# Performance work log

Hardware: AMD Instinct MI355X
Metric: run time of the kernel (lower is better)

Reference implementation:

```python
import jax, jax.numpy as jnp
import numpy as np

B, VN, QN, KN = 64, 100, 64, 64
V_DIM, Q_DIM, KG_DIM = 2048, 768, 300
H_DIM, RANK, GLIMPSE = 1024, 32, 2
HD = H_DIM // RANK  # 32


def setup_inputs() -> dict:
    key = jax.random.key(0)
    ks = jax.random.split(key, 10)
    v = jax.random.normal(ks[0], (B, VN, V_DIM), jnp.float32)
    # zero out last 10 regions so the padding mask path is exercised
    v = v.at[:, VN - 10:, :].set(0.0)
    q = jax.random.normal(ks[1], (B, QN, Q_DIM), jnp.float32)
    kg = jax.random.normal(ks[2], (B, KN, KG_DIM), jnp.float32)
    s = lambda d: 1.0 / np.sqrt(d)
    Wv = jax.random.normal(ks[3], (V_DIM, H_DIM), jnp.float32) * s(V_DIM)
    bv = jnp.zeros((H_DIM,), jnp.float32)
    Wq = jax.random.normal(ks[4], (Q_DIM, H_DIM), jnp.float32) * s(Q_DIM)
    bq = jnp.zeros((H_DIM,), jnp.float32)
    Wkg = jax.random.normal(ks[5], (KG_DIM, H_DIM), jnp.float32) * s(KG_DIM)
    bkg = jnp.zeros((H_DIM,), jnp.float32)
    # core tensor (torch init is normal_(); scaled down so softmax isn't saturated)
    T_g = jax.random.normal(ks[6], (1, RANK, HD, HD, HD, GLIMPSE), jnp.float32) * 0.02
    return {"v": v, "q": q, "kg": kg, "Wv": Wv, "bv": bv, "Wq": Wq, "bq": bq,
            "Wkg": Wkg, "bkg": bkg, "T_g": T_g}


def _tri_logits(v, q, kg, Wv, bv, Wq, bq, Wkg, bkg, T_g):
    b, vn = v.shape[:2]
    qn, kn = q.shape[1], kg.shape[1]
    rank, hd, g = T_g.shape[1], T_g.shape[2], T_g.shape[-1]
    fc = lambda x, W, bb: jax.nn.relu(x @ W + bb)  # FCNet (weight-norm Linear + ReLU), eval: no dropout
    # project to h_dim and split into `rank` contiguous chunks of size hd -> [R,B,N,hd]
    vt = jnp.transpose(fc(v, Wv, bv).reshape(b, vn, rank, hd), (2, 0, 1, 3))
    qt = jnp.transpose(fc(q, Wq, bq).reshape(b, qn, rank, hd), (2, 0, 1, 3))
    kt = jnp.transpose(fc(kg, Wkg, bkg).reshape(b, kn, rank, hd), (2, 0, 1, 3))

    def step(acc, xs):
        vr, qr, kr, Tr = xs  # [B,V,hd],[B,Q,hd],[B,K,hd],[hd,hd,hd,g]
        t = jnp.einsum('bvx,xyzg->bvyzg', vr, Tr)
        t = jnp.einsum('bvyzg,bqy->bvqzg', t, qr)
        t = jnp.einsum('bvqzg,bkz->bvqkg', t, kr)
        return acc + t, None

    init = jnp.zeros((b, vn, qn, kn, g), v.dtype)
    logits, _ = jax.lax.scan(step, init, (vt, qt, kt, T_g[0]))
    return logits  # [B,V,Q,K,glimpse]


def reference(v, q, kg, Wv, bv, Wq, bq, Wkg, bkg, T_g):
    b, vn = v.shape[:2]
    qn, kn = q.shape[1], kg.shape[1]
    g = T_g.shape[-1]
    logits = _tri_logits(v, q, kg, Wv, bv, Wq, bq, Wkg, bkg, T_g)
    # mask padded image regions (all-zero feature rows)
    mask = jnp.sum(jnp.abs(v), axis=2) == 0  # [B,V]
    logits = jnp.where(mask[:, :, None, None, None], -jnp.inf, logits)
    # softmax over the flattened V*Q*K axis, per glimpse
    p = jax.nn.softmax(logits.reshape(b, vn * qn * kn, g), axis=1)
    return p.reshape(b, vn, qn, kn, g), logits
```

## Files before the change

### kernel.cpp

```cpp
#include <hip/hip_runtime.h>
#include <cstdint>
#include <math.h>

#define MASK_VAL (-1e30f)

#define Bb   64
#define VN   100
#define QN   64
#define KN   64
#define VD   2048
#define QD   768
#define KGD  300
#define KGP  320
#define HH   1024
#define RR   32
#define HDm  32
#define GG   2
#define NBV  (Bb*VN)
#define LOGN ((size_t)NBV*QN*KN*GG)

typedef _Float16 half_t;
typedef _Float16 f16x8 __attribute__((ext_vector_type(8)));
typedef _Float16 f16x4 __attribute__((ext_vector_type(4)));
typedef float    f32x4 __attribute__((ext_vector_type(4)));

#define MFMA_F16(a,b,c) __builtin_amdgcn_mfma_f32_16x16x32_f16(a,b,c,0,0,0)

#define PN0 13107200
#define PN1 3145728
#define PN2 1310720
#define PN3 2097152
#define PN4 786432
#define PN5 327680
#define PN6 2097152
#define PTOT (PN0+PN1+PN2+PN3+PN4+PN5+PN6)

__device__ inline void fm_decode(long d, int KB, int& row, int& k) {
  int blk = (int)(d >> 9);
  int lc = (int)((d >> 7) & 3), lr = (int)((d >> 3) & 15), h = (int)(d & 7);
  row = (blk / KB) * 16 + lr;
  k   = (blk % KB) * 32 + lc*8 + h;
}

__global__ __launch_bounds__(256) void preproc_kernel(const float* __restrict__ v,
                                                      const float* __restrict__ q,
                                                      const float* __restrict__ kg,
                                                      const float* __restrict__ Wv,
                                                      const float* __restrict__ Wq,
                                                      const float* __restrict__ Wkg,
                                                      const float* __restrict__ Tg,
                                                      half_t* __restrict__ v16,
                                                      half_t* __restrict__ q16,
                                                      half_t* __restrict__ k16,
                                                      half_t* __restrict__ Wvt,
                                                      half_t* __restrict__ Wqt,
                                                      half_t* __restrict__ Wkt,
                                                      half_t* __restrict__ Tpp)
{
  long idx = (long)blockIdx.x*256 + threadIdx.x;
  if (idx >= PTOT) return;
  int row, k;
  if (idx < PN0) { fm_decode(idx, 64, row, k); v16[idx] = (half_t)v[(size_t)row*VD + k]; return; }
  idx -= PN0;
  if (idx < PN1) { fm_decode(idx, 24, row, k); q16[idx] = (half_t)q[(size_t)row*QD + k]; return; }
  idx -= PN1;
  if (idx < PN2) {
    fm_decode(idx, 10, row, k);
    k16[idx] = (half_t)((k < KGD) ? kg[(size_t)row*KGD + k] : 0.f);
    return;
  }
  idx -= PN2;
  if (idx < PN3) { fm_decode(idx, 64, row, k); Wvt[idx] = (half_t)Wv[(size_t)k*HH + row]; return; }
  idx -= PN3;
  if (idx < PN4) { fm_decode(idx, 24, row, k); Wqt[idx] = (half_t)Wq[(size_t)k*HH + row]; return; }
  idx -= PN4;
  if (idx < PN5) {
    fm_decode(idx, 10, row, k);
    Wkt[idx] = (half_t)((k < KGD) ? Wkg[(size_t)k*HH + row] : 0.f);
    return;
  }
  idx -= PN5;
  {
    int r = (int)(idx >> 16), rem = (int)(idx & 65535);
    int cp = rem >> 5, x = rem & 31;
    int y = cp & 31, zg = cp >> 5;
    Tpp[idx + (size_t)0] = (half_t)Tg[((size_t)(r*32 + x) << 11) + y*64 + zg];
  }
}

__global__ __launch_bounds__(256) void mask_kernel(const float* __restrict__ v,
                                                   float* __restrict__ maskv)
{
  int row = blockIdx.x;
  int tid = threadIdx.x;
  const float* src = v + (size_t)row * VD;
  float s = 0.f;
  for (int i = tid; i < VD/4; i += 256) {
    float4 x = *(const float4*)&src[i*4];
    s += fabsf(x.x)+fabsf(x.y)+fabsf(x.z)+fabsf(x.w);
  }
#pragma unroll
  for (int off=32; off; off>>=1) s += __shfl_down(s, off);
  __shared__ float red[4];
  if ((tid & 63) == 0) red[tid>>6] = s;
  __syncthreads();
  if (tid == 0) maskv[row] = ((red[0]+red[1]+red[2]+red[3]) == 0.f) ? 1.f : 0.f;
}

__global__ __launch_bounds__(256) void proj_mfma_kernel(const half_t* __restrict__ A0,
                                                        const half_t* __restrict__ A1,
                                                        const half_t* __restrict__ A2,
                                                        const half_t* __restrict__ W0,
                                                        const half_t* __restrict__ W1,
                                                        const half_t* __restrict__ W2,
                                                        const float* __restrict__ b0p,
                                                        const float* __restrict__ b1p,
                                                        const float* __restrict__ b2p,
                                                        half_t* __restrict__ H0,
                                                        half_t* __restrict__ H1,
                                                        half_t* __restrict__ H2)
{
  int z = blockIdx.z;
  int Mb = (z == 0) ? 100 : 64;
  if ((int)blockIdx.x >= Mb) return;
  const half_t* A  = (z==0) ? A0 : (z==1) ? A1 : A2;
  const half_t* Wt = (z==0) ? W0 : (z==1) ? W1 : W2;
  const float* bias = (z==0) ? b0p : (z==1) ? b1p : b2p;
  half_t* H = (z==0) ? H0 : (z==1) ? H1 : H2;
  int KB = (z==0) ? 64 : (z==1) ? 24 : 10;

  int w = threadIdx.x >> 6, lane = threadIdx.x & 63;
  int mtile = blockIdx.x*4 + w;
  int n0 = blockIdx.y*64;
  int lr = lane & 15, lc = lane >> 4;
  f32x4 acc[4];
#pragma unroll
  for (int nt=0;nt<4;nt++) acc[nt] = (f32x4)(0.f);
  const half_t* abase = A + ((size_t)mtile*KB)*512 + lane*8;
  const half_t* wbase = Wt + ((size_t)(blockIdx.y*4)*KB)*512 + lane*8;
  for (int kb = 0; kb < KB; kb++) {
    f16x8 a = *(const f16x8*)(abase + (size_t)kb*512);
#pragma unroll
    for (int nt = 0; nt < 4; nt++) {
      f16x8 b = *(const f16x8*)(wbase + ((size_t)nt*KB + kb)*512);
      acc[nt] = MFMA_F16(a, b, acc[nt]);
    }
  }
  int m0 = mtile*16;
#pragma unroll
  for (int nt = 0; nt < 4; nt++) {
    float bb = bias[n0 + nt*16 + lr];
#pragma unroll
    for (int j = 0; j < 4; j++) {
      float vv = fmaxf(acc[nt][j] + bb, 0.f);
      H[(size_t)(m0 + lc*4 + j)*HH + n0 + nt*16 + lr] = (half_t)vv;
    }
  }
}

__global__ __launch_bounds__(256) void stageA_mfma_kernel(const half_t* __restrict__ hv,
                                                          const half_t* __restrict__ Tpp,
                                                          half_t* __restrict__ u, int r0)
{
  __shared__ half_t tile[4][16][256];
  int rc = blockIdx.z; int r = r0 + rc;
  int w = threadIdx.x >> 6, lane = threadIdx.x & 63;
  int m0 = blockIdx.x*64 + w*16;
  int n0 = blockIdx.y*256;
  int lr = lane & 15, lc = lane >> 4;
  f16x8 bH = *(const f16x8*)(hv + (size_t)(m0 + lr)*HH + r*HDm + lc*8);
  const half_t* ta = Tpp + ((size_t)r << 16) + (size_t)n0*32 + lr*32 + lc*8;
  half_t* myt = &tile[w][0][0];
#pragma unroll
  for (int t = 0; t < 16; t++) {
    f16x8 aT = *(const f16x8*)(ta + t*512);
    f32x4 d = MFMA_F16(aT, bH, (f32x4)(0.f));
    f16x4 pk;
    pk[0] = (half_t)d[0]; pk[1] = (half_t)d[1];
    pk[2] = (half_t)d[2]; pk[3] = (half_t)d[3];
    int col4 = (t*4 + lc) ^ (lr & 14);
    *(f16x4*)(myt + lr*256 + col4*4) = pk;
  }
  half_t* ub = u + ((size_t)rc*NBV + m0)*2048 + n0;
  int hl = lane >> 5;
  int cc = lane & 31;
#pragma unroll
  for (int i = 0; i < 8; i++) {
    int rrow = i*2 + hl;
    int pc4 = (cc*2) ^ (rrow & 14);
    f16x8 val = *(const f16x8*)(myt + rrow*256 + pc4*4);
    *(f16x8*)(ub + (size_t)rrow*2048 + cc*8) = val;
  }
}

#define WSTRIDE 2080
__global__ __launch_bounds__(256,2) void triBC_mfma_kernel(const half_t* __restrict__ hq,
                                                           const half_t* __restrict__ hk,
                                                           const half_t* __restrict__ u,
                                                           const float* __restrict__ maskv,
                                                           uint32_t* __restrict__ logits16,
                                                           float* __restrict__ pm,
                                                           float* __restrict__ ps,
                                                           int r0, int RC, int isFirst, int isLast)
{
  __shared__ __align__(16) half_t qtf[2][2048];
  __shared__ __align__(16) half_t ktf[2][2048];
  __shared__ __align__(16) half_t wsm[4*2*WSTRIDE];
  int tid = threadIdx.x;
  int w = tid >> 6, lane = tid & 63;
  half_t* wme = wsm + w*(2*WSTRIDE);
  int vt = blockIdx.x, b = blockIdx.y;
  int bv = b*VN + vt*4 + w;
  int lr = lane & 15, lc = lane >> 4;

  f32x4 acc[2][4][4];
#pragma unroll
  for (int g=0;g<2;g++)
#pragma unroll
    for (int mt=0;mt<4;mt++)
#pragma unroll
      for (int nt=0;nt<4;nt++) acc[g][mt][nt] = (f32x4)(0.f);

  int srow = tid >> 2, sch = tid & 3;
  const half_t* qsrc = hq + (size_t)(b*QN + srow)*HH + sch*8;
  const half_t* ksrc = hk + (size_t)(b*KN + srow)*HH + sch*8;
  int sdst = (srow>>4)*512 + ((srow&15) + sch*16)*8;
  const half_t* ulane = u + (size_t)bv*2048 + lr*HDm + lc*8;

  *(f16x8*)&qtf[0][sdst] = *(const f16x8*)(qsrc + r0*HDm);
  *(f16x8*)&ktf[0][sdst] = *(const f16x8*)(ksrc + r0*HDm);
  int rp1 = (RC > 1) ? 1 : 0;
  f16x8 qhold = *(const f16x8*)(qsrc + (r0+rp1)*HDm);
  f16x8 khold = *(const f16x8*)(ksrc + (r0+rp1)*HDm);
  f16x8 ub[4];
#pragma unroll
  for (int nt=0;nt<4;nt++) ub[nt] = *(const f16x8*)(ulane + nt*512);
  asm volatile("s_waitcnt lgkmcnt(0)" ::: "memory");
  __builtin_amdgcn_s_barrier();

  for (int rc = 0; rc < RC; rc++) {
    int bp = rc & 1;
    int rn1 = (rc+1 < RC) ? rc+1 : RC-1;
    int rn2 = (rc+2 < RC) ? rc+2 : RC-1;
    f16x8 qa[4], bk[4];
#pragma unroll
    for (int mt=0;mt<4;mt++) qa[mt] = *(const f16x8*)&qtf[bp][mt*512 + lane*8];
#pragma unroll
    for (int nt=0;nt<4;nt++) bk[nt] = *(const f16x8*)&ktf[bp][nt*512 + lane*8];
    *(f16x8*)&qtf[bp^1][sdst] = qhold;
    *(f16x8*)&ktf[bp^1][sdst] = khold;
    qhold = *(const f16x8*)(qsrc + (r0+rn2)*HDm);
    khold = *(const f16x8*)(ksrc + (r0+rn2)*HDm);
    f16x8 ubN[4];
#pragma unroll
    for (int nt=0;nt<4;nt++)
      ubN[nt] = *(const f16x8*)(ulane + (size_t)rn1*NBV*2048 + nt*512);
#pragma unroll
    for (int nt=0;nt<4;nt++) {
      f32x4 wv[4];
#pragma unroll
      for (int mt=0;mt<4;mt++) wv[mt] = MFMA_F16(qa[mt], ub[nt], (f32x4)(0.f));
#pragma unroll
      for (int mt=0;mt<4;mt++) {
#pragma unroll
        for (int j=0;j<4;j++) {
          int dst = (lr&1)*WSTRIDE + mt*512 + (lc*4 + j + nt*16)*8 + (lr>>1);
          wme[dst] = (half_t)wv[mt][j];
        }
      }
    }
#pragma unroll
    for (int g=0;g<2;g++) {
      f16x8 am[4];
#pragma unroll
      for (int mt=0;mt<4;mt++) am[mt] = *(const f16x8*)&wme[g*WSTRIDE + mt*512 + lane*8];
#pragma unroll
      for (int mt=0;mt<4;mt++)
#pragma unroll
        for (int nt=0;nt<4;nt++)
          acc[g][mt][nt] = MFMA_F16(am[mt], bk[nt], acc[g][mt][nt]);
    }
    asm volatile("s_waitcnt lgkmcnt(0)" ::: "memory");
    __builtin_amdgcn_s_barrier();
#pragma unroll
    for (int nt=0;nt<4;nt++) ub[nt] = ubN[nt];
  }

  float mk = maskv[bv];
  uint32_t* lb16 = logits16 + (size_t)bv*QN*KN;
#pragma unroll
  for (int mt=0;mt<4;mt++)
#pragma unroll
    for (int nt=0;nt<4;nt++)
#pragma unroll
      for (int j=0;j<4;j++) {
        size_t off = (size_t)(mt*16 + lc*4 + j)*KN + nt*16 + lr;
        float g0 = acc[0][mt][nt][j], g1 = acc[1][mt][nt][j];
        if (!isFirst) {
          union { uint32_t u32; half_t h[2]; } pv;
          pv.u32 = lb16[off];
          g0 += (float)pv.h[0]; g1 += (float)pv.h[1];
        }
        if (isLast && mk != 0.f) { g0 = MASK_VAL; g1 = MASK_VAL; }
        union { uint32_t u32; half_t h[2]; } pk;
        pk.h[0] = (half_t)g0; pk.h[1] = (half_t)g1;
        lb16[off] = pk.u32;
        acc[0][mt][nt][j] = g0; acc[1][mt][nt][j] = g1;
      }
  if (isLast) {
#pragma unroll
    for (int g=0; g<2; g++) {
      float mloc = acc[g][0][0][0];
#pragma unroll
      for (int mt=0;mt<4;mt++)
#pragma unroll
        for (int nt=0;nt<4;nt++)
#pragma unroll
          for (int j=0;j<4;j++) mloc = fmaxf(mloc, acc[g][mt][nt][j]);
      float sloc = 0.f;
#pragma unroll
      for (int mt=0;mt<4;mt++)
#pragma unroll
        for (int nt=0;nt<4;nt++)
#pragma unroll
          for (int j=0;j<4;j++) sloc += __expf(acc[g][mt][nt][j] - mloc);
#pragma unroll
      for (int off2=1; off2<64; off2<<=1) {
        float m2 = __shfl_xor(mloc, off2);
        float s2 = __shfl_xor(sloc, off2);
        float mn = fmaxf(mloc, m2);
        sloc = sloc*__expf(mloc-mn) + s2*__expf(m2-mn);
        mloc = mn;
      }
      if (lane == 0) { pm[(size_t)bv*GG + g] = mloc; ps[(size_t)bv*GG + g] = sloc; }
    }
  }
}

__global__ __launch_bounds__(64) void combine_kernel(const float* __restrict__ pm,
                                                     const float* __restrict__ ps,
                                                     float* __restrict__ Mg, float* __restrict__ Sg)
{
  int bg = blockIdx.x; int b = bg >> 1, g = bg & 1;
  int lane = threadIdx.x;
  float m = pm[((size_t)b*VN + lane)*GG + g];
  float s = ps[((size_t)b*VN + lane)*GG + g];
  if (lane + 64 < VN) {
    float m2 = pm[((size_t)b*VN + lane + 64)*GG + g];
    float s2 = ps[((size_t)b*VN + lane + 64)*GG + g];
    float mn = fmaxf(m, m2);
    s = s*__expf(m-mn) + s2*__expf(m2-mn); m = mn;
  }
#pragma unroll
  for (int off=1; off<64; off<<=1) {
    float m2 = __shfl_xor(m, off);
    float s2 = __shfl_xor(s, off);
    float mn = fmaxf(m, m2);
    s = s*__expf(m-mn) + s2*__expf(m2-mn);
    m = mn;
  }
  if (lane == 0) { Mg[b*GG+g] = m; Sg[b*GG+g] = s; }
}

__global__ __launch_bounds__(256) void pwrite16_kernel(const uint32_t* __restrict__ lg,
                                                       const float* __restrict__ Mg,
                                                       const float* __restrict__ Sg,
                                                       float* __restrict__ p)
{
  const size_t PER_B = (size_t)VN*QN*KN;
  const size_t n2 = LOGN/4;
  size_t stride = (size_t)gridDim.x * 256;
  for (size_t t = (size_t)blockIdx.x*256 + threadIdx.x; t < n2; t += stride) {
    size_t i0 = t*2;
    int b = (int)(i0 / PER_B);
    float M0 = Mg[b*2], M1 = Mg[b*2+1];
    float iS0 = 1.f/Sg[b*2], iS1 = 1.f/Sg[b*2+1];
    union { uint2 v; half_t h[4]; } x;
    x.v = *(const uint2*)&lg[i0];
    float4 o;
    o.x = __expf((float)x.h[0] - M0)*iS0;
    o.y = __expf((float)x.h[1] - M1)*iS1;
    o.z = __expf((float)x.h[2] - M0)*iS0;
    o.w = __expf((float)x.h[3] - M1)*iS1;
    *(float4*)&p[i0*2] = o;
  }
}

extern "C" void kernel_launch(void* const* d_in, const int* in_sizes, int n_in,
                              void* d_out, int out_size, void* d_ws, size_t ws_size,
                              hipStream_t stream)
{
  const float* v   = (const float*)d_in[0];
  const float* q   = (const float*)d_in[1];
  const float* kg  = (const float*)d_in[2];
  const float* Wv  = (const float*)d_in[3];
  const float* bv  = (const float*)d_in[4];
  const float* Wq  = (const float*)d_in[5];
  const float* bq  = (const float*)d_in[6];
  const float* Wkg = (const float*)d_in[7];
  const float* bkg = (const float*)d_in[8];
  const float* Tg  = (const float*)d_in[9];
  float* p_out  = (float*)d_out;
  uint32_t* logits16 = (uint32_t*)(p_out + LOGN);

  char* ws = (char*)d_ws;
  size_t off = 0;
  auto alloc = [&](size_t bytes) -> char* {
    char* ptr = ws + off;
    off = (off + bytes + 255) & ~(size_t)255;
    return ptr;
  };
  half_t* h_v16 = (half_t*)alloc((size_t)NBV*HH*2);
  half_t* h_q16 = (half_t*)alloc((size_t)Bb*QN*HH*2);
  half_t* h_k16 = (half_t*)alloc((size_t)Bb*KN*HH*2);
  half_t* v16   = (half_t*)alloc((size_t)NBV*VD*2);
  half_t* q16   = (half_t*)alloc((size_t)Bb*QN*QD*2);
  half_t* k16   = (half_t*)alloc((size_t)Bb*KN*KGP*2);
  half_t* Wvt   = (half_t*)alloc((size_t)HH*VD*2);
  half_t* Wqt   = (half_t*)alloc((size_t)HH*QD*2);
  half_t* Wkt   = (half_t*)alloc((size_t)HH*KGP*2);
  half_t* Tpp   = (half_t*)alloc((size_t)32*65536*2);
  float* maskv  = (float*)alloc((size_t)NBV*4);
  float* pm     = (float*)alloc((size_t)NBV*GG*4);
  float* ps     = (float*)alloc((size_t)NBV*GG*4);
  float* Mg     = (float*)alloc(128*4);
  float* Sg     = (float*)alloc(128*4);
  size_t WS_FIXED = off;
  const size_t USZB = (size_t)NBV*2048*2;

  int RC; half_t* u;
  if      (WS_FIXED + 32*USZB <= ws_size) { RC = 32; u = (half_t*)(ws + off); }
  else if (WS_FIXED + 16*USZB <= ws_size) { RC = 16; u = (half_t*)(ws + off); }
  else if (WS_FIXED +  8*USZB <= ws_size) { RC =  8; u = (half_t*)(ws + off); }
  else { RC = 8; u = (half_t*)p_out; }

  preproc_kernel<<<(unsigned)((PTOT + 255)/256),256,0,stream>>>(v, q, kg, Wv, Wq, Wkg, Tg,
                                                                v16, q16, k16, Wvt, Wqt, Wkt, Tpp);
  mask_kernel<<<NBV,256,0,stream>>>(v, maskv);

  proj_mfma_kernel<<<dim3(100,16,3),256,0,stream>>>(v16, q16, k16, Wvt, Wqt, Wkt,
                                                    bv, bq, bkg, h_v16, h_q16, h_k16);

  for (int r0 = 0; r0 < RR; r0 += RC) {
    stageA_mfma_kernel<<<dim3(100,8,RC),256,0,stream>>>(h_v16, Tpp, u, r0);
    triBC_mfma_kernel<<<dim3(25,Bb),256,0,stream>>>(h_q16, h_k16, u, maskv, logits16, pm, ps,
                                                    r0, RC, (r0==0)?1:0, (r0+RC>=RR)?1:0);
  }
  combine_kernel<<<128,64,0,stream>>>(pm, ps, Mg, Sg);
  pwrite16_kernel<<<2048,256,0,stream>>>(logits16, Mg, Sg, p_out);
}
```

Before: 725.0 us.

## Skip tri-linear MFMA work for masked regions and restructure W staging layout

Reads the padding mask up front. Blocks whose four regions are all masked exit early after writing the masked logits and softmax partials. Individual masked waves skip their loads and MFMAs but still join the barriers. The intermediate W tile is also produced with swapped MFMA operands and packed as paired halves in a new uint32 LDS layout, aiming to cut per-element LDS stores. The risk is that the new layout has to match the fragment order the second MFMA expects.

```diff
diff --git a/kernel.cpp b/kernel.cpp
--- a/kernel.cpp
+++ b/kernel.cpp
@@ -193,7 +193,6 @@
   }
 }
 
-#define WSTRIDE 2080
 __global__ __launch_bounds__(256,2) void triBC_mfma_kernel(const half_t* __restrict__ hq,
                                                            const half_t* __restrict__ hk,
                                                            const half_t* __restrict__ u,
@@ -205,13 +204,37 @@
 {
   __shared__ __align__(16) half_t qtf[2][2048];
   __shared__ __align__(16) half_t ktf[2][2048];
-  __shared__ __align__(16) half_t wsm[4*2*WSTRIDE];
+  __shared__ uint32_t wlds[4][2048];
   int tid = threadIdx.x;
   int w = tid >> 6, lane = tid & 63;
-  half_t* wme = wsm + w*(2*WSTRIDE);
+  uint32_t* wme = wlds[w];
   int vt = blockIdx.x, b = blockIdx.y;
   int bv = b*VN + vt*4 + w;
   int lr = lane & 15, lc = lane >> 4;
+
+  int bvb = b*VN + vt*4;
+  float mk0 = maskv[bvb+0], mk1 = maskv[bvb+1], mk2 = maskv[bvb+2], mk3 = maskv[bvb+3];
+  bool myMasked = ((w==0?mk0 : w==1?mk1 : w==2?mk2 : mk3) != 0.f);
+  bool allMasked = (mk0!=0.f) && (mk1!=0.f) && (mk2!=0.f) && (mk3!=0.f);
+  if (allMasked) {
+    if (isLast) {
+      union { uint32_t u32; half_t h[2]; } pk;
+      pk.h[0] = (half_t)MASK_VAL; pk.h[1] = (half_t)MASK_VAL;
+      uint32_t* lb16 = logits16 + (size_t)bv*QN*KN;
+#pragma unroll
+      for (int mt=0;mt<4;mt++)
+#pragma unroll
+        for (int nt=0;nt<4;nt++)
+#pragma unroll
+          for (int j=0;j<4;j++)
+            lb16[(size_t)(mt*16 + lc*4 + j)*KN + nt*16 + lr] = pk.u32;
+      if (lane == 0) {
+        pm[(size_t)bv*GG+0] = MASK_VAL; ps[(size_t)bv*GG+0] = 4096.f;
+        pm[(size_t)bv*GG+1] = MASK_VAL; ps[(size_t)bv*GG+1] = 4096.f;
+      }
+    }
+    return;
+  }
 
   f32x4 acc[2][4][4];
 #pragma unroll
@@ -233,8 +256,10 @@
   f16x8 qhold = *(const f16x8*)(qsrc + (r0+rp1)*HDm);
   f16x8 khold = *(const f16x8*)(ksrc + (r0+rp1)*HDm);
   f16x8 ub[4];
-#pragma unroll
-  for (int nt=0;nt<4;nt++) ub[nt] = *(const f16x8*)(ulane + nt*512);
+  if (!myMasked) {
+#pragma unroll
+    for (int nt=0;nt<4;nt++) ub[nt] = *(const f16x8*)(ulane + nt*512);
+  }
   asm volatile("s_waitcnt lgkmcnt(0)" ::: "memory");
   __builtin_amdgcn_s_barrier();
 
@@ -242,52 +267,70 @@
     int bp = rc & 1;
     int rn1 = (rc+1 < RC) ? rc+1 : RC-1;
     int rn2 = (rc+2 < RC) ? rc+2 : RC-1;
-    f16x8 qa[4], bk[4];
-#pragma unroll
-    for (int mt=0;mt<4;mt++) qa[mt] = *(const f16x8*)&qtf[bp][mt*512 + lane*8];
-#pragma unroll
-    for (int nt=0;nt<4;nt++) bk[nt] = *(const f16x8*)&ktf[bp][nt*512 + lane*8];
     *(f16x8*)&qtf[bp^1][sdst] = qhold;
     *(f16x8*)&ktf[bp^1][sdst] = khold;
     qhold = *(const f16x8*)(qsrc + (r0+rn2)*HDm);
     khold = *(const f16x8*)(ksrc + (r0+rn2)*HDm);
-    f16x8 ubN[4];
-#pragma unroll
-    for (int nt=0;nt<4;nt++)
-      ubN[nt] = *(const f16x8*)(ulane + (size_t)rn1*NBV*2048 + nt*512);
-#pragma unroll
-    for (int nt=0;nt<4;nt++) {
-      f32x4 wv[4];
-#pragma unroll
-      for (int mt=0;mt<4;mt++) wv[mt] = MFMA_F16(qa[mt], ub[nt], (f32x4)(0.f));
-#pragma unroll
-      for (int mt=0;mt<4;mt++) {
-#pragma unroll
-        for (int j=0;j<4;j++) {
-          int dst = (lr&1)*WSTRIDE + mt*512 + (lc*4 + j + nt*16)*8 + (lr>>1);
-          wme[dst] = (half_t)wv[mt][j];
+    if (!myMasked) {
+      f16x8 qa[4], bk[4];
+#pragma unroll
+      for (int mt=0;mt<4;mt++) qa[mt] = *(const f16x8*)&qtf[bp][mt*512 + lane*8];
+#pragma unroll
+      for (int nt=0;nt<4;nt++) bk[nt] = *(const f16x8*)&ktf[bp][nt*512 + lane*8];
+      f16x8 ubN[4];
+#pragma unroll
+      for (int nt=0;nt<4;nt++)
+        ubN[nt] = *(const f16x8*)(ulane + (size_t)rn1*NBV*2048 + nt*512);
+#pragma unroll
+      for (int t=0;t<4;t++) {
+#pragma unroll
+        for (int mt=0;mt<4;mt++) {
+          f32x4 d = MFMA_F16(ub[t], qa[mt], (f32x4)(0.f));
+          union { uint32_t u32; half_t h[2]; } p0, p1;
+          p0.h[0] = (half_t)d[0]; p0.h[1] = (half_t)d[2];
+          p1.h[0] = (half_t)d[1]; p1.h[1] = (half_t)d[3];
+          wme[(t*8 + 0*4 + mt)*64 + lr*4 + lc] = p0.u32;
+          wme[(t*8 + 1*4 + mt)*64 + lr*4 + lc] = p1.u32;
         }
       }
-    }
-#pragma unroll
-    for (int g=0;g<2;g++) {
-      f16x8 am[4];
-#pragma unroll
-      for (int mt=0;mt<4;mt++) am[mt] = *(const f16x8*)&wme[g*WSTRIDE + mt*512 + lane*8];
-#pragma unroll
-      for (int mt=0;mt<4;mt++)
-#pragma unroll
-        for (int nt=0;nt<4;nt++)
-          acc[g][mt][nt] = MFMA_F16(am[mt], bk[nt], acc[g][mt][nt]);
+#pragma unroll
+      for (int g=0;g<2;g++) {
+        f16x8 am[4];
+#pragma unroll
+        for (int mt=0;mt<4;mt++)
+          am[mt] = *(const f16x8*)&wme[(lc*8 + g*4 + mt)*64 + lr*4];
+#pragma unroll
+        for (int mt=0;mt<4;mt++)
+#pragma unroll
+          for (int nt=0;nt<4;nt++)
+            acc[g][mt][nt] = MFMA_F16(am[mt], bk[nt], acc[g][mt][nt]);
+      }
+#pragma unroll
+      for (int nt=0;nt<4;nt++) ub[nt] = ubN[nt];
     }
     asm volatile("s_waitcnt lgkmcnt(0)" ::: "memory");
     __builtin_amdgcn_s_barrier();
-#pragma unroll
-    for (int nt=0;nt<4;nt++) ub[nt] = ubN[nt];
-  }
-
-  float mk = maskv[bv];
+  }
+
   uint32_t* lb16 = logits16 + (size_t)bv*QN*KN;
+  if (myMasked) {
+    if (isLast) {
+      union { uint32_t u32; half_t h[2]; } pk;
+      pk.h[0] = (half_t)MASK_VAL; pk.h[1] = (half_t)MASK_VAL;
+#pragma unroll
+      for (int mt=0;mt<4;mt++)
+#pragma unroll
+        for (int nt=0;nt<4;nt++)
+#pragma unroll
+          for (int j=0;j<4;j++)
+            lb16[(size_t)(mt*16 + lc*4 + j)*KN + nt*16 + lr] = pk.u32;
+      if (lane == 0) {
+        pm[(size_t)bv*GG+0] = MASK_VAL; ps[(size_t)bv*GG+0] = 4096.f;
+        pm[(size_t)bv*GG+1] = MASK_VAL; ps[(size_t)bv*GG+1] = 4096.f;
+      }
+    }
+    return;
+  }
 #pragma unroll
   for (int mt=0;mt<4;mt++)
 #pragma unroll
@@ -301,7 +344,6 @@
           pv.u32 = lb16[off];
           g0 += (float)pv.h[0]; g1 += (float)pv.h[1];
         }
-        if (isLast && mk != 0.f) { g0 = MASK_VAL; g1 = MASK_VAL; }
         union { uint32_t u32; half_t h[2]; } pk;
         pk.h[0] = (half_t)g0; pk.h[1] = (half_t)g1;
         lb16[off] = pk.u32;
```

Result: faster. 671.2 us (-7.4%).
